# Optimization experiments

Hardware: AMD Instinct MI355X
Metric: run time of the kernel (lower is better)

The kernel has to match this reference:

```python
import jax, jax.numpy as jnp
import numpy as np

D_MODEL = 1024
RANK = 256
N_HEADS = 8
D_HEAD = RANK // N_HEADS
N_COMPRESS = 64
N_EXPAND = 64
N_KNOWLEDGE = 8192
COMPRESS_TOP_K = 8
EXPAND_TOP_K = 4
KNOWLEDGE_K = 8
B, S = 4, 512
NEG_INF = -1e9


def setup_inputs() -> dict:
    key = jax.random.key(0)
    ks = jax.random.split(key, 12)
    inp = {
        'x': jax.random.normal(ks[0], (B, S, D_MODEL), jnp.float32),
        'mask': jnp.tril(jnp.ones((S, S), bool))[None, None],  # [1,1,S,S] causal
        'compress_neurons': jax.random.normal(ks[1], (N_COMPRESS, D_MODEL, RANK), jnp.float32) / np.sqrt(D_MODEL),
        'expand_neurons': jax.random.normal(ks[2], (N_EXPAND, RANK, D_MODEL), jnp.float32) / np.sqrt(RANK),
        'knowledge_K': jax.random.normal(ks[3], (N_KNOWLEDGE, RANK), jnp.float32) * 0.02,
        'knowledge_V': jax.random.normal(ks[4], (N_KNOWLEDGE, D_MODEL), jnp.float32) * 0.02,
        'rq_w': jax.random.normal(ks[5], (N_COMPRESS, D_MODEL), jnp.float32) / np.sqrt(D_MODEL),
        'rk_w': jax.random.normal(ks[6], (N_COMPRESS, D_MODEL), jnp.float32) / np.sqrt(D_MODEL),
        'rv_w': jax.random.normal(ks[7], (N_COMPRESS, D_MODEL), jnp.float32) / np.sqrt(D_MODEL),
        'ro_w': jax.random.normal(ks[8], (N_EXPAND, RANK), jnp.float32) / np.sqrt(RANK),
        'rm_w': jax.random.normal(ks[9], (N_COMPRESS, D_MODEL), jnp.float32) / np.sqrt(D_MODEL),
        'g1': jnp.ones((D_MODEL,), jnp.float32),
        'b1': jnp.zeros((D_MODEL,), jnp.float32),
        'g2': jnp.ones((D_MODEL,), jnp.float32),
        'b2': jnp.zeros((D_MODEL,), jnp.float32),
    }
    return inp


def layernorm(x, g, b, eps=1e-5):
    mu = jnp.mean(x, -1, keepdims=True)
    var = jnp.mean((x - mu) ** 2, -1, keepdims=True)
    return (x - mu) * jax.lax.rsqrt(var + eps) * g + b


def compress(x, router_w, neurons, top_k):
    # x: [B,S,D]; neurons: [N,D,R]. Gather-then-matmul == matmul-then-gather.
    scores = jnp.einsum('bsd,nd->bsn', x, router_w)
    topk_scores, topk_idx = jax.lax.top_k(scores, top_k)
    w = jax.nn.softmax(topk_scores, -1)                          # [B,S,k]
    proj = jnp.einsum('bsd,ndr->bsnr', x, neurons)               # [B,S,N,R]
    sel = jnp.take_along_axis(proj, topk_idx[..., None], axis=2)  # [B,S,k,R]
    return jnp.sum(sel * w[..., None], axis=2)                   # [B,S,R]


def expand(x, router_w, neurons, top_k):
    # x: [B,S,R]; neurons: [N,R,D]
    scores = jnp.einsum('bsr,nr->bsn', x, router_w)
    topk_scores, topk_idx = jax.lax.top_k(scores, top_k)
    w = jax.nn.softmax(topk_scores, -1)
    proj = jnp.einsum('bsr,nrd->bsnd', x, neurons)               # [B,S,N,D]
    sel = jnp.take_along_axis(proj, topk_idx[..., None], axis=2)  # [B,S,k,D]
    return jnp.sum(sel * w[..., None], axis=2)                   # [B,S,D]


def reference(x, mask, compress_neurons, expand_neurons, knowledge_K, knowledge_V,
              rq_w, rk_w, rv_w, ro_w, rm_w, g1, b1, g2, b2):
    b, s, d = x.shape
    # --- attention sub-block (NeuronCircuit), pre-LN residual ---
    h = layernorm(x, g1, b1)
    Q = compress(h, rq_w, compress_neurons, COMPRESS_TOP_K)
    K = compress(h, rk_w, compress_neurons, COMPRESS_TOP_K)
    V = compress(h, rv_w, compress_neurons, COMPRESS_TOP_K)
    Q = Q.reshape(b, s, N_HEADS, D_HEAD).transpose(0, 2, 1, 3)
    K = K.reshape(b, s, N_HEADS, D_HEAD).transpose(0, 2, 1, 3)
    V = V.reshape(b, s, N_HEADS, D_HEAD).transpose(0, 2, 1, 3)
    att = jnp.einsum('bhqd,bhkd->bhqk', Q, K) / np.sqrt(D_HEAD)
    att = jnp.where(mask, att, NEG_INF)
    att = jax.nn.softmax(att, -1)
    attn_out = jnp.einsum('bhqk,bhkd->bhqd', att, V)
    attn_out = attn_out.transpose(0, 2, 1, 3).reshape(b, s, RANK)
    attn_out = expand(attn_out, ro_w, expand_neurons, EXPAND_TOP_K)
    x1 = x + attn_out
    # --- memory sub-block (NeuronMemory) ---
    h2 = layernorm(x1, g2, b2)
    Qm = compress(h2, rm_w, compress_neurons, COMPRESS_TOP_K)    # [B,S,R]
    kscores = jnp.einsum('bsr,nr->bsn', Qm, knowledge_K) / np.sqrt(RANK)
    k_top, k_idx = jax.lax.top_k(kscores, KNOWLEDGE_K)
    kw = jax.nn.softmax(k_top, -1)                               # [B,S,kk]
    sel_V = knowledge_V[k_idx]                                   # [B,S,kk,D]
    mem_out = jnp.sum(sel_V * kw[..., None], axis=2)
    return x1 + mem_out
```

## Files before the change

### kernel.cpp

```cpp
#include <hip/hip_runtime.h>

#define BS   2048
#define DM   1024
#define RK   256
#define NKN  8192
#define CK   8
#define EK   4
#define KK   8
#define KCH  32

#define NEGINF -1e30f

typedef __attribute__((ext_vector_type(8))) short short8;
typedef __attribute__((ext_vector_type(4))) float f32x4;

__device__ __forceinline__ unsigned short bf16_rtn(float v) {
  unsigned bits = __float_as_uint(v);
  return (unsigned short)((bits + 0x7fffu + ((bits >> 16) & 1u)) >> 16);
}
__device__ __forceinline__ float bf16f(unsigned short u) {
  return __uint_as_float(((unsigned)u) << 16);
}
__device__ __forceinline__ void split2(float v, unsigned short& h, unsigned short& l) {
  h = bf16_rtn(v);
  l = bf16_rtn(v - bf16f(h));
}

template<int TOPK>
__device__ inline void wave_topk64(float bv, int lane, float* tops, int* tidx) {
  #pragma unroll
  for (int k = 0; k < TOPK; ++k) {
    float mv = bv; int mp = lane;
    #pragma unroll
    for (int off = 32; off > 0; off >>= 1) {
      float ov = __shfl_xor(mv, off); int op = __shfl_xor(mp, off);
      if (ov > mv || (ov == mv && op < mp)) { mv = ov; mp = op; }
    }
    tops[k] = mv; tidx[k] = mp;
    if (lane == mp) bv = NEGINF;
  }
}

template<int TOPK>
__device__ inline void router_commit(int token, const float* tops, const int* tidx,
    float* w_out, int* lists, int* counts) {
  float mx = tops[0], se = 0.f, ex[TOPK];
  #pragma unroll
  for (int k = 0; k < TOPK; ++k) { ex[k] = expf(tops[k] - mx); se += ex[k]; }
  float inv = 1.f / se;
  #pragma unroll
  for (int k = 0; k < TOPK; ++k) {
    w_out[token*TOPK + k] = ex[k] * inv;
    int pos = atomicAdd(&counts[tidx[k]], 1);
    lists[tidx[k]*BS + pos] = token*TOPK + k;
  }
}

__global__ __launch_bounds__(256) void cvt_rwT(const float* __restrict__ rw,
                                               float* __restrict__ rwT, int dim4) {
  int i = blockIdx.x*256 + threadIdx.x;
  if (i >= 64*dim4) return;
  int n = i / dim4, jg = i % dim4;
  float4 v = *reinterpret_cast<const float4*>(rw + (size_t)n*dim4*4 + jg*4);
  *reinterpret_cast<float4*>(rwT + (size_t)jg*256 + n*4) = v;
}

__global__ __launch_bounds__(256) void ln_router3(const float* __restrict__ xin,
    const float* __restrict__ g, const float* __restrict__ bb,
    unsigned short* __restrict__ hh, unsigned short* __restrict__ hl,
    const float* __restrict__ w0T, const float* __restrict__ w1T, const float* __restrict__ w2T,
    float* __restrict__ w_all, int* __restrict__ lists, int* __restrict__ counts) {
  int row = blockIdx.x, t = threadIdx.x;
  __shared__ float red[256];
  __shared__ __align__(16) float hrow[DM];
  __shared__ float part[3][4][64];
  const float4 v = *reinterpret_cast<const float4*>(xin + (size_t)row*DM + t*4);
  red[t] = v.x + v.y + v.z + v.w;
  __syncthreads();
  for (int o = 128; o > 0; o >>= 1) { if (t < o) red[t] += red[t+o]; __syncthreads(); }
  float mu = red[0] * (1.f/DM);
  __syncthreads();
  float dx = v.x-mu, dy = v.y-mu, dz = v.z-mu, dw = v.w-mu;
  red[t] = dx*dx + dy*dy + dz*dz + dw*dw;
  __syncthreads();
  for (int o = 128; o > 0; o >>= 1) { if (t < o) red[t] += red[t+o]; __syncthreads(); }
  float rs = rsqrtf(red[0]*(1.f/DM) + 1e-5f);
  float4 gv = *reinterpret_cast<const float4*>(g + t*4);
  float4 bv = *reinterpret_cast<const float4*>(bb + t*4);
  float4 o4 = make_float4(dx*rs*gv.x+bv.x, dy*rs*gv.y+bv.y, dz*rs*gv.z+bv.z, dw*rs*gv.w+bv.w);
  ushort4 uh, ul;
  split2(o4.x, uh.x, ul.x); split2(o4.y, uh.y, ul.y);
  split2(o4.z, uh.z, ul.z); split2(o4.w, uh.w, ul.w);
  *reinterpret_cast<ushort4*>(hh + (size_t)row*DM + t*4) = uh;
  *reinterpret_cast<ushort4*>(hl + (size_t)row*DM + t*4) = ul;
  *reinterpret_cast<float4*>(&hrow[t*4]) = o4;
  __syncthreads();
  int n = t & 63, c = t >> 6;
  const float4* b0p = reinterpret_cast<const float4*>(w0T) + (size_t)c*64*64 + n;
  const float4* b1p = reinterpret_cast<const float4*>(w1T) + (size_t)c*64*64 + n;
  const float4* b2p = reinterpret_cast<const float4*>(w2T) + (size_t)c*64*64 + n;
  float p0 = 0.f, p1 = 0.f, p2 = 0.f;
  #pragma unroll 8
  for (int jg = 0; jg < 64; ++jg) {
    float4 a  = *reinterpret_cast<const float4*>(&hrow[(c*64 + jg)*4]);
    float4 b0 = b0p[(size_t)jg*64];
    float4 b1 = b1p[(size_t)jg*64];
    float4 b2 = b2p[(size_t)jg*64];
    p0 += a.x*b0.x + a.y*b0.y + a.z*b0.z + a.w*b0.w;
    p1 += a.x*b1.x + a.y*b1.y + a.z*b1.z + a.w*b1.w;
    p2 += a.x*b2.x + a.y*b2.y + a.z*b2.z + a.w*b2.w;
  }
  part[0][c][n] = p0; part[1][c][n] = p1; part[2][c][n] = p2;
  __syncthreads();
  int wv = t >> 6, lane = t & 63;
  if (wv < 3) {
    float bvv = part[wv][0][lane] + part[wv][1][lane] + part[wv][2][lane] + part[wv][3][lane];
    float tops[CK]; int tidx[CK];
    wave_topk64<CK>(bvv, lane, tops, tidx);
    if (lane == 0)
      router_commit<CK>(row, tops, tidx, w_all + (size_t)wv*BS*CK,
                        lists + (size_t)wv*64*BS, counts + wv*64);
  }
}

__global__ __launch_bounds__(256) void ln_router1(const float* __restrict__ xin,
    const float* __restrict__ g, const float* __restrict__ bb,
    unsigned short* __restrict__ hh, unsigned short* __restrict__ hl,
    const float* __restrict__ rwT,
    float* __restrict__ w_out, int* __restrict__ lists, int* __restrict__ counts) {
  int row = blockIdx.x, t = threadIdx.x;
  __shared__ float red[256];
  __shared__ __align__(16) float hrow[DM];
  __shared__ float part[4][64];
  const float4 v = *reinterpret_cast<const float4*>(xin + (size_t)row*DM + t*4);
  red[t] = v.x + v.y + v.z + v.w;
  __syncthreads();
  for (int o = 128; o > 0; o >>= 1) { if (t < o) red[t] += red[t+o]; __syncthreads(); }
  float mu = red[0] * (1.f/DM);
  __syncthreads();
  float dx = v.x-mu, dy = v.y-mu, dz = v.z-mu, dw = v.w-mu;
  red[t] = dx*dx + dy*dy + dz*dz + dw*dw;
  __syncthreads();
  for (int o = 128; o > 0; o >>= 1) { if (t < o) red[t] += red[t+o]; __syncthreads(); }
  float rs = rsqrtf(red[0]*(1.f/DM) + 1e-5f);
  float4 gv = *reinterpret_cast<const float4*>(g + t*4);
  float4 bv = *reinterpret_cast<const float4*>(bb + t*4);
  float4 o4 = make_float4(dx*rs*gv.x+bv.x, dy*rs*gv.y+bv.y, dz*rs*gv.z+bv.z, dw*rs*gv.w+bv.w);
  ushort4 uh, ul;
  split2(o4.x, uh.x, ul.x); split2(o4.y, uh.y, ul.y);
  split2(o4.z, uh.z, ul.z); split2(o4.w, uh.w, ul.w);
  *reinterpret_cast<ushort4*>(hh + (size_t)row*DM + t*4) = uh;
  *reinterpret_cast<ushort4*>(hl + (size_t)row*DM + t*4) = ul;
  *reinterpret_cast<float4*>(&hrow[t*4]) = o4;
  __syncthreads();
  int n = t & 63, c = t >> 6;
  const float4* bp = reinterpret_cast<const float4*>(rwT) + (size_t)c*64*64 + n;
  float p = 0.f;
  #pragma unroll 8
  for (int jg = 0; jg < 64; ++jg) {
    float4 a = *reinterpret_cast<const float4*>(&hrow[(c*64 + jg)*4]);
    float4 b = bp[(size_t)jg*64];
    p += a.x*b.x + a.y*b.y + a.z*b.z + a.w*b.w;
  }
  part[c][n] = p;
  __syncthreads();
  if (t < 64) {
    float bvv = part[0][t] + part[1][t] + part[2][t] + part[3][t];
    float tops[CK]; int tidx[CK];
    wave_topk64<CK>(bvv, t, tops, tidx);
    if (t == 0) router_commit<CK>(row, tops, tidx, w_out, lists, counts);
  }
}

template<int DIM, int TOPK>
__global__ __launch_bounds__(256) void router_topkT(const float* __restrict__ xin,
    const float* __restrict__ rwT, float* __restrict__ w_out,
    int* __restrict__ lists, int* __restrict__ counts) {
  int token = blockIdx.x, t = threadIdx.x;
  __shared__ __align__(16) float xrow[DIM];
  __shared__ float part[4][64];
  for (int i = t; i < DIM/4; i += 256)
    *reinterpret_cast<float4*>(&xrow[i*4]) =
        *reinterpret_cast<const float4*>(xin + (size_t)token*DIM + i*4);
  __syncthreads();
  int n = t & 63, c = t >> 6;
  const int JG = DIM / 16;
  const float4* bp = reinterpret_cast<const float4*>(rwT) + (size_t)c*JG*64 + n;
  float p = 0.f;
  #pragma unroll 8
  for (int jg = 0; jg < JG; ++jg) {
    float4 a = *reinterpret_cast<const float4*>(&xrow[(c*JG + jg)*4]);
    float4 b = bp[(size_t)jg*64];
    p += a.x*b.x + a.y*b.y + a.z*b.z + a.w*b.w;
  }
  part[c][n] = p;
  __syncthreads();
  if (t < 64) {
    float bv = part[0][t] + part[1][t] + part[2][t] + part[3][t];
    float tops[TOPK]; int tidx[TOPK];
    wave_topk64<TOPK>(bv, t, tops, tidx);
    if (t == 0) router_commit<TOPK>(token, tops, tidx, w_out, lists, counts);
  }
}

__global__ __launch_bounds__(256) void cvt_cnT(const float* __restrict__ cn,
    unsigned short* __restrict__ th, unsigned short* __restrict__ tl) {
  __shared__ float tile[32][33];
  int kb = blockIdx.x*32, cb = blockIdx.y*32, e = blockIdx.z;
  int tx = threadIdx.x & 31, ty = threadIdx.x >> 5;
  const size_t ebase = (size_t)e * DM * RK;
  for (int r = ty; r < 32; r += 8)
    tile[r][tx] = cn[ebase + (size_t)(kb + r)*RK + cb + tx];
  __syncthreads();
  for (int r = ty; r < 32; r += 8) {
    float v = tile[tx][r];
    unsigned short h, l; split2(v, h, l);
    size_t o = (size_t)e*RK*DM + (size_t)(cb + r)*DM + kb + tx;
    th[o] = h; tl[o] = l;
  }
}

__global__ __launch_bounds__(256) void ggemm_mfma(
    const unsigned short* __restrict__ xh, const unsigned short* __restrict__ xl,
    const unsigned short* __restrict__ WTh, const unsigned short* __restrict__ WTl,
    const float* __restrict__ w_all, const int* __restrict__ lists,
    const int* __restrict__ counts, float* __restrict__ out) {
  int e = blockIdx.x, which = blockIdx.z;
  int cnt = counts[which*64 + e];
  int base = blockIdx.y * 64;
  if (base >= cnt) return;
  const int* list_e = lists + ((size_t)which*64 + e)*BS;
  const float* wvp = w_all + (size_t)which*BS*CK;
  int t = threadIdx.x, w = t >> 6, l = t & 63, lr = l & 15, lg = l >> 4;
  __shared__ int   toks[64];
  __shared__ float wts[64];
  if (t < 64) {
    int idx = base + t;
    if (idx < cnt) { int e2 = list_e[idx]; toks[t] = e2 / CK; wts[t] = wvp[e2]; }
    else           { toks[t] = -1; wts[t] = 0.f; }
  }
  __syncthreads();
  f32x4 acc[4][4];
  #pragma unroll
  for (int mi = 0; mi < 4; ++mi)
    #pragma unroll
    for (int ni = 0; ni < 4; ++ni) acc[mi][ni] = (f32x4)0.f;
  const unsigned short* Ahb = WTh + ((size_t)e*RK + w*64 + lr)*DM + lg*8;
  const unsigned short* Alb = WTl + ((size_t)e*RK + w*64 + lr)*DM + lg*8;
  int tokn[4]; float wtn[4];
  const unsigned short *Bh[4], *Bl[4];
  #pragma unroll
  for (int ni = 0; ni < 4; ++ni) {
    tokn[ni] = toks[ni*16 + lr];
    wtn[ni]  = wts[ni*16 + lr];
    int tk = tokn[ni] >= 0 ? tokn[ni] : 0;
    Bh[ni] = xh + (size_t)tk*DM + lg*8;
    Bl[ni] = xl + (size_t)tk*DM + lg*8;
  }
  for (int k0 = 0; k0 < DM; k0 += 32) {
    short8 ah[4], al[4], bh[4], bl[4];
    #pragma unroll
    for (int mi = 0; mi < 4; ++mi) {
      ah[mi] = *reinterpret_cast<const short8*>(Ahb + (size_t)mi*16*DM + k0);
      al[mi] = *reinterpret_cast<const short8*>(Alb + (size_t)mi*16*DM + k0);
    }
    #pragma unroll
    for (int ni = 0; ni < 4; ++ni) {
      bh[ni] = *reinterpret_cast<const short8*>(Bh[ni] + k0);
      bl[ni] = *reinterpret_cast<const short8*>(Bl[ni] + k0);
    }
    #pragma unroll
    for (int mi = 0; mi < 4; ++mi)
      #pragma unroll
      for (int ni = 0; ni < 4; ++ni) {
        acc[mi][ni] = __builtin_amdgcn_mfma_f32_16x16x32_bf16(ah[mi], bh[ni], acc[mi][ni], 0, 0, 0);
        acc[mi][ni] = __builtin_amdgcn_mfma_f32_16x16x32_bf16(ah[mi], bl[ni], acc[mi][ni], 0, 0, 0);
        acc[mi][ni] = __builtin_amdgcn_mfma_f32_16x16x32_bf16(al[mi], bh[ni], acc[mi][ni], 0, 0, 0);
      }
  }
  #pragma unroll
  for (int ni = 0; ni < 4; ++ni) {
    if (tokn[ni] < 0) continue;
    float wt = wtn[ni];
    float* orow = out + ((size_t)which*BS + tokn[ni])*RK;
    #pragma unroll
    for (int mi = 0; mi < 4; ++mi) {
      int col = w*64 + mi*16 + lg*4;
      #pragma unroll
      for (int r = 0; r < 4; ++r)
        atomicAdd(&orow[col + r], wt * acc[mi][ni][r]);
    }
  }
}

template<int KDIM, int NCOLT, int TK>
__global__ __launch_bounds__(256) void ggemm_f32(const float* __restrict__ xin,
    const float* __restrict__ neurons, const float* __restrict__ w_all,
    const int* __restrict__ lists, const int* __restrict__ counts,
    float* __restrict__ out) {
  constexpr int COLCH = NCOLT / 256;
  int e = blockIdx.x;
  int which = blockIdx.z / COLCH, cc = blockIdx.z % COLCH;
  int cnt = counts[which*64 + e];
  int base = blockIdx.y * 64;
  if (base >= cnt) return;
  const int* list_e = lists + ((size_t)which*64 + e)*BS;
  const float* wvp = w_all + (size_t)which*BS*TK;
  int t = threadIdx.x;
  __shared__ __align__(16) float Bs[16][256];
  __shared__ __align__(16) float At[16][64];
  __shared__ int   toks[64];
  __shared__ float wts[64];
  if (t < 64) {
    int idx = base + t;
    if (idx < cnt) { int e2 = list_e[idx]; toks[t] = e2 / TK; wts[t] = wvp[e2]; }
    else           { toks[t] = -1; wts[t] = 0.f; }
  }
  __syncthreads();
  float acc[8][8];
  #pragma unroll
  for (int i = 0; i < 8; ++i)
    #pragma unroll
    for (int j = 0; j < 8; ++j) acc[i][j] = 0.f;
  int tr = t >> 5, tc = t & 31;
  const float* W = neurons + (size_t)e*KDIM*NCOLT + cc*256;
  int ar = t & 63, akc = (t >> 6) * 4;
  int tokA = toks[ar];
  const float* Arow = xin + (size_t)(tokA >= 0 ? tokA : 0)*KDIM + akc;

  for (int k0 = 0; k0 < KDIM; k0 += 16) {
    float4 b0r, b1r, b2r, b3r;
    {
      int f0 = t*4;
      b0r = *reinterpret_cast<const float4*>(W + (size_t)(k0 + (f0>>8))*NCOLT + (f0&255));
      int f1 = 1024 + t*4;
      b1r = *reinterpret_cast<const float4*>(W + (size_t)(k0 + (f1>>8))*NCOLT + (f1&255));
      int f2 = 2048 + t*4;
      b2r = *reinterpret_cast<const float4*>(W + (size_t)(k0 + (f2>>8))*NCOLT + (f2&255));
      int f3 = 3072 + t*4;
      b3r = *reinterpret_cast<const float4*>(W + (size_t)(k0 + (f3>>8))*NCOLT + (f3&255));
    }
    float4 av = *reinterpret_cast<const float4*>(Arow + k0);
    if (tokA < 0) av = make_float4(0.f, 0.f, 0.f, 0.f);
    __syncthreads();
    {
      int f0 = t*4;
      *reinterpret_cast<float4*>(&Bs[0][0] + f0)        = b0r;
      *reinterpret_cast<float4*>(&Bs[0][0] + f0 + 1024) = b1r;
      *reinterpret_cast<float4*>(&Bs[0][0] + f0 + 2048) = b2r;
      *reinterpret_cast<float4*>(&Bs[0][0] + f0 + 3072) = b3r;
      At[akc+0][ar] = av.x; At[akc+1][ar] = av.y;
      At[akc+2][ar] = av.z; At[akc+3][ar] = av.w;
    }
    __syncthreads();
    #pragma unroll
    for (int kk = 0; kk < 16; ++kk) {
      float4 a0 = *reinterpret_cast<const float4*>(&At[kk][tr*8]);
      float4 a1 = *reinterpret_cast<const float4*>(&At[kk][tr*8 + 4]);
      float4 p0 = *reinterpret_cast<const float4*>(&Bs[kk][tc*4]);
      float4 p1 = *reinterpret_cast<const float4*>(&Bs[kk][128 + tc*4]);
      float a[8] = {a0.x,a0.y,a0.z,a0.w,a1.x,a1.y,a1.z,a1.w};
      float b[8] = {p0.x,p0.y,p0.z,p0.w,p1.x,p1.y,p1.z,p1.w};
      #pragma unroll
      for (int i = 0; i < 8; ++i)
        #pragma unroll
        for (int j = 0; j < 8; ++j)
          acc[i][j] = fmaf(a[i], b[j], acc[i][j]);
    }
  }
  #pragma unroll
  for (int i = 0; i < 8; ++i) {
    int r = tr*8 + i;
    int tok = toks[r];
    if (tok < 0) continue;
    float wt = wts[r];
    float* orow = out + ((size_t)which*BS + tok)*NCOLT + cc*256;
    #pragma unroll
    for (int j = 0; j < 4; ++j) {
      atomicAdd(&orow[tc*4 + j],       wt * acc[i][j]);
      atomicAdd(&orow[128 + tc*4 + j], wt * acc[i][j+4]);
    }
  }
}

__global__ __launch_bounds__(256) void attn_kernel(const float* __restrict__ Q,
    const float* __restrict__ K, const float* __restrict__ V, float* __restrict__ AO) {
  int qs = blockIdx.x;
  int hb = blockIdx.y; int h = hb & 7, b = hb >> 3;
  int t = threadIdx.x;
  __shared__ float qv[32];
  __shared__ float sc[512];
  __shared__ float red[256];
  const size_t baseQ = ((size_t)(b*512 + qs))*RK + h*32;
  if (t < 32) qv[t] = Q[baseQ + t];
  __syncthreads();
  int nk = qs + 1;
  const float scale = 0.17677669529663687f;
  for (int k = t; k < nk; k += 256) {
    const float* kr = K + ((size_t)(b*512 + k))*RK + h*32;
    float s = 0.f;
    #pragma unroll
    for (int d = 0; d < 32; d += 4) {
      float4 kv = *reinterpret_cast<const float4*>(kr + d);
      s += kv.x*qv[d] + kv.y*qv[d+1] + kv.z*qv[d+2] + kv.w*qv[d+3];
    }
    sc[k] = s * scale;
  }
  __syncthreads();
  float m = NEGINF;
  for (int k = t; k < nk; k += 256) m = fmaxf(m, sc[k]);
  red[t] = m; __syncthreads();
  for (int o = 128; o > 0; o >>= 1) { if (t < o) red[t] = fmaxf(red[t], red[t+o]); __syncthreads(); }
  m = red[0];
  __syncthreads();
  float sloc = 0.f;
  for (int k = t; k < nk; k += 256) { float pp = expf(sc[k] - m); sc[k] = pp; sloc += pp; }
  red[t] = sloc; __syncthreads();
  for (int o = 128; o > 0; o >>= 1) { if (t < o) red[t] += red[t+o]; __syncthreads(); }
  float inv = 1.f / red[0];
  __syncthreads();
  int d = t & 31, c = t >> 5;
  float pa = 0.f;
  for (int k = c; k < nk; k += 8)
    pa += sc[k] * V[((size_t)(b*512 + k))*RK + h*32 + d];
  red[c*32 + d] = pa; __syncthreads();
  if (t < 32) {
    float o = 0.f;
    #pragma unroll
    for (int c2 = 0; c2 < 8; ++c2) o += red[c2*32 + t];
    AO[baseQ + t] = o * inv;
  }
}

__global__ __launch_bounds__(256) void f2bf(const float* __restrict__ in,
                                            unsigned short* __restrict__ out, int n8) {
  int i = blockIdx.x*256 + threadIdx.x;
  if (i >= n8) return;
  float4 a = reinterpret_cast<const float4*>(in)[2*i];
  float4 b = reinterpret_cast<const float4*>(in)[2*i + 1];
  float v[8] = {a.x,a.y,a.z,a.w,b.x,b.y,b.z,b.w};
  unsigned u[8];
  #pragma unroll
  for (int j = 0; j < 8; ++j) {
    unsigned bits = __float_as_uint(v[j]);
    u[j] = (bits + 0x7fffu + ((bits >> 16) & 1u)) >> 16;
  }
  uint4 o;
  o.x = u[0] | (u[1] << 16); o.y = u[2] | (u[3] << 16);
  o.z = u[4] | (u[5] << 16); o.w = u[6] | (u[7] << 16);
  *reinterpret_cast<uint4*>(out + 8*i) = o;
}

__global__ __launch_bounds__(256) void kscore_mfma(const unsigned short* __restrict__ Qmb,
    const unsigned short* __restrict__ kKb, float* __restrict__ cand_s, int* __restrict__ cand_i) {
  int tile = blockIdx.x, chunk = blockIdx.y;
  int t = threadIdx.x, w = t >> 6, l = t & 63;
  int lr = l & 15, lg = l >> 4;
  __shared__ float sc[32][265];
  f32x4 acc[4][2];
  #pragma unroll
  for (int mi = 0; mi < 4; ++mi)
    #pragma unroll
    for (int ti = 0; ti < 2; ++ti) acc[mi][ti] = (f32x4)0.f;
  const unsigned short* Abase = kKb + ((size_t)(chunk*256 + w*64 + lr))*RK + lg*8;
  const unsigned short* Bbase = Qmb + ((size_t)(tile*32 + lr))*RK + lg*8;
  #pragma unroll
  for (int k0 = 0; k0 < RK; k0 += 32) {
    short8 af[4], bf[2];
    #pragma unroll
    for (int mi = 0; mi < 4; ++mi)
      af[mi] = *reinterpret_cast<const short8*>(Abase + (size_t)mi*16*RK + k0);
    #pragma unroll
    for (int ti = 0; ti < 2; ++ti)
      bf[ti] = *reinterpret_cast<const short8*>(Bbase + (size_t)ti*16*RK + k0);
    #pragma unroll
    for (int mi = 0; mi < 4; ++mi)
      #pragma unroll
      for (int ti = 0; ti < 2; ++ti)
        acc[mi][ti] = __builtin_amdgcn_mfma_f32_16x16x32_bf16(af[mi], bf[ti], acc[mi][ti], 0, 0, 0);
  }
  #pragma unroll
  for (int mi = 0; mi < 4; ++mi)
    #pragma unroll
    for (int ti = 0; ti < 2; ++ti)
      #pragma unroll
      for (int r = 0; r < 4; ++r)
        sc[ti*16 + lr][w*64 + mi*16 + lg*4 + r] = acc[mi][ti][r];
  __syncthreads();
  for (int s = 0; s < 8; ++s) {
    int tok = w*8 + s;
    float v0 = sc[tok][l], v1 = sc[tok][l+64], v2 = sc[tok][l+128], v3 = sc[tok][l+192];
    size_t cbase = ((size_t)(tile*32 + tok)*KCH + chunk)*KK;
    #pragma unroll
    for (int iter = 0; iter < KK; ++iter) {
      float mv = v0; int mp = l;
      if (v1 > mv) { mv = v1; mp = l+64; }
      if (v2 > mv) { mv = v2; mp = l+128; }
      if (v3 > mv) { mv = v3; mp = l+192; }
      #pragma unroll
      for (int off = 32; off > 0; off >>= 1) {
        float ov = __shfl_xor(mv, off); int op = __shfl_xor(mp, off);
        if (ov > mv || (ov == mv && op < mp)) { mv = ov; mp = op; }
      }
      if ((mp & 63) == l) {
        int j = mp >> 6;
        if (j == 0) v0 = NEGINF; else if (j == 1) v1 = NEGINF;
        else if (j == 2) v2 = NEGINF; else v3 = NEGINF;
      }
      if (l == 0) { cand_s[cbase + iter] = mv; cand_i[cbase + iter] = chunk*256 + mp; }
    }
  }
}

__global__ __launch_bounds__(256) void knowledge_merge(const float* __restrict__ cand_s,
    const int* __restrict__ cand_i, const float* __restrict__ kV, float* __restrict__ xout) {
  int tok = blockIdx.x, t = threadIdx.x;
  __shared__ float s_sc[256];
  __shared__ int   s_ix[256];
  __shared__ float w8[KK];
  __shared__ int   i8[KK];
  s_sc[t] = cand_s[(size_t)tok*256 + t];
  s_ix[t] = cand_i[(size_t)tok*256 + t];
  __syncthreads();
  if (t < 64) {
    float v0 = s_sc[t], v1 = s_sc[t+64], v2 = s_sc[t+128], v3 = s_sc[t+192];
    float tops[KK]; int tpos[KK];
    #pragma unroll
    for (int iter = 0; iter < KK; ++iter) {
      float mv = v0; int mp = t;
      if (v1 > mv) { mv = v1; mp = t+64; }
      if (v2 > mv) { mv = v2; mp = t+128; }
      if (v3 > mv) { mv = v3; mp = t+192; }
      #pragma unroll
      for (int off = 32; off > 0; off >>= 1) {
        float ov = __shfl_xor(mv, off); int op = __shfl_xor(mp, off);
        if (ov > mv || (ov == mv && op < mp)) { mv = ov; mp = op; }
      }
      tops[iter] = mv; tpos[iter] = mp;
      if ((mp & 63) == t) {
        int j = mp >> 6;
        if (j == 0) v0 = NEGINF; else if (j == 1) v1 = NEGINF;
        else if (j == 2) v2 = NEGINF; else v3 = NEGINF;
      }
    }
    if (t == 0) {
      const float kscale = 1.f/16.f;
      float mx = tops[0]*kscale, se = 0.f, ex[KK];
      #pragma unroll
      for (int k = 0; k < KK; ++k) { ex[k] = expf(tops[k]*kscale - mx); se += ex[k]; }
      float inv = 1.f / se;
      #pragma unroll
      for (int k = 0; k < KK; ++k) { w8[k] = ex[k]*inv; i8[k] = s_ix[tpos[k]]; }
    }
  }
  __syncthreads();
  size_t orow = (size_t)tok * DM;
  float4 o = *reinterpret_cast<const float4*>(xout + orow + t*4);
  #pragma unroll
  for (int k = 0; k < KK; ++k) {
    float w = w8[k];
    const float4 v4 = *reinterpret_cast<const float4*>(kV + (size_t)i8[k]*DM + t*4);
    o.x += w*v4.x; o.y += w*v4.y; o.z += w*v4.z; o.w += w*v4.w;
  }
  *reinterpret_cast<float4*>(xout + orow + t*4) = o;
}

extern "C" void kernel_launch(void* const* d_in, const int* in_sizes, int n_in,
                              void* d_out, int out_size, void* d_ws, size_t ws_size,
                              hipStream_t stream) {
  const float* x  = (const float*)d_in[0];
  const float* cn = (const float*)d_in[2];
  const float* en = (const float*)d_in[3];
  const float* kK = (const float*)d_in[4];
  const float* kV = (const float*)d_in[5];
  const float* rq = (const float*)d_in[6];
  const float* rk = (const float*)d_in[7];
  const float* rv = (const float*)d_in[8];
  const float* ro = (const float*)d_in[9];
  const float* rm = (const float*)d_in[10];
  const float* g1 = (const float*)d_in[11];
  const float* b1 = (const float*)d_in[12];
  const float* g2 = (const float*)d_in[13];
  const float* b2 = (const float*)d_in[14];
  float* out = (float*)d_out;

  char* p = (char*)d_ws;
  auto alloc = [&](size_t bytes) { char* r = p; p += (bytes + 255) & ~(size_t)255; return r; };
  unsigned short* h_h  = (unsigned short*)alloc((size_t)BS*DM*2);
  unsigned short* h_l  = (unsigned short*)alloc((size_t)BS*DM*2);
  unsigned short* h2_h = (unsigned short*)alloc((size_t)BS*DM*2);
  unsigned short* h2_l = (unsigned short*)alloc((size_t)BS*DM*2);
  unsigned short* cnT_h = (unsigned short*)alloc((size_t)64*RK*DM*2);
  unsigned short* cnT_l = (unsigned short*)alloc((size_t)64*RK*DM*2);
  float* rqT  = (float*)alloc((size_t)64*DM*4);
  float* rkT  = (float*)alloc((size_t)64*DM*4);
  float* rvT  = (float*)alloc((size_t)64*DM*4);
  float* rmT  = (float*)alloc((size_t)64*DM*4);
  float* roT  = (float*)alloc((size_t)64*RK*4);
  float* Q    = (float*)alloc((size_t)BS*RK*4);
  float* Kb   = (float*)alloc((size_t)BS*RK*4);
  float* Vb   = (float*)alloc((size_t)BS*RK*4);
  float* Qm   = (float*)alloc((size_t)BS*RK*4);
  float* AO   = (float*)alloc((size_t)BS*RK*4);
  float* w_all= (float*)alloc((size_t)3*BS*CK*4);
  float* w_o  = (float*)alloc((size_t)BS*EK*4);
  float* w_m  = (float*)alloc((size_t)BS*CK*4);
  float* cand_s = (float*)alloc((size_t)BS*KCH*KK*4);
  int*   cand_i = (int*)  alloc((size_t)BS*KCH*KK*4);
  unsigned short* Qmb = (unsigned short*)alloc((size_t)BS*RK*2);
  unsigned short* kKb = (unsigned short*)alloc((size_t)NKN*RK*2);
  int* lists  = (int*)alloc((size_t)5*64*BS*4);
  int* counts = (int*)alloc((size_t)5*64*4);

  int *listo = lists + 3*64*BS, *listm = lists + 4*64*BS;
  int *co = counts + 192, *cm = counts + 256;

  hipMemsetAsync(counts, 0, 5*64*4, stream);
  hipMemsetAsync(Q, 0, (size_t)BS*RK*4*4, stream);

  cvt_rwT<<<64, 256, 0, stream>>>(rq, rqT, DM/4);
  cvt_rwT<<<64, 256, 0, stream>>>(rk, rkT, DM/4);
  cvt_rwT<<<64, 256, 0, stream>>>(rv, rvT, DM/4);
  cvt_rwT<<<64, 256, 0, stream>>>(rm, rmT, DM/4);
  cvt_rwT<<<16, 256, 0, stream>>>(ro, roT, RK/4);
  cvt_cnT<<<dim3(32, 8, 64), 256, 0, stream>>>(cn, cnT_h, cnT_l);
  f2bf<<<NKN*RK/8/256, 256, 0, stream>>>(kK, kKb, NKN*RK/8);

  ln_router3<<<BS, 256, 0, stream>>>(x, g1, b1, h_h, h_l, rqT, rkT, rvT, w_all, lists, counts);
  ggemm_mfma<<<dim3(64, 16, 3), 256, 0, stream>>>(h_h, h_l, cnT_h, cnT_l,
                                                  w_all, lists, counts, Q);

  attn_kernel<<<dim3(512, 32), 256, 0, stream>>>(Q, Kb, Vb, AO);

  hipMemcpyAsync(out, x, (size_t)BS*DM*4, hipMemcpyDeviceToDevice, stream);

  router_topkT<RK, EK><<<BS, 256, 0, stream>>>(AO, roT, w_o, listo, co);
  ggemm_f32<RK, DM, EK><<<dim3(64, 16, 4), 256, 0, stream>>>(AO, en, w_o, listo, co, out);

  ln_router1<<<BS, 256, 0, stream>>>(out, g2, b2, h2_h, h2_l, rmT, w_m, listm, cm);
  ggemm_mfma<<<dim3(64, 16, 1), 256, 0, stream>>>(h2_h, h2_l, cnT_h, cnT_l,
                                                  w_m, listm, cm, Qm);

  f2bf<<<BS*RK/8/256, 256, 0, stream>>>(Qm, Qmb, BS*RK/8);
  kscore_mfma<<<dim3(BS/32, KCH), 256, 0, stream>>>(Qmb, kKb, cand_s, cand_i);
  knowledge_merge<<<BS, 256, 0, stream>>>(cand_s, cand_i, kV, out);
}
```

Measured before the change: 1.437 ms.

## Merge Q/K/V router lists per expert so one grouped GEMM tile serves all three

The three compress routers (Q, K, V) now write into a single per-expert list with a shared counter, and each entry encodes which projection it belongs to. The grouped MFMA GEMM then reads one combined list per expert rather than three separate lists. This packs tokens from all three projections into full 64-row tiles and reuses each expert's weight tile across them, so fewer blocks run partially filled. In exchange, the atomic counter per expert sees three times the contention and the token index has to be decoded with bit tricks.

```diff
diff --git a/kernel.cpp b/kernel.cpp
--- a/kernel.cpp
+++ b/kernel.cpp
@@ -8,6 +8,7 @@
 #define EK   4
 #define KK   8
 #define KCH  32
+#define LSTR (3*BS)
 
 #define NEGINF -1e30f
 
@@ -43,7 +44,7 @@
 
 template<int TOPK>
 __device__ inline void router_commit(int token, const float* tops, const int* tidx,
-    float* w_out, int* lists, int* counts) {
+    float* w_out, int entoff, int* lists, int lstr, int* counts) {
   float mx = tops[0], se = 0.f, ex[TOPK];
   #pragma unroll
   for (int k = 0; k < TOPK; ++k) { ex[k] = expf(tops[k] - mx); se += ex[k]; }
@@ -52,7 +53,7 @@
   for (int k = 0; k < TOPK; ++k) {
     w_out[token*TOPK + k] = ex[k] * inv;
     int pos = atomicAdd(&counts[tidx[k]], 1);
-    lists[tidx[k]*BS + pos] = token*TOPK + k;
+    lists[tidx[k]*lstr + pos] = entoff + token*TOPK + k;
   }
 }
 
@@ -69,7 +70,7 @@
     const float* __restrict__ g, const float* __restrict__ bb,
     unsigned short* __restrict__ hh, unsigned short* __restrict__ hl,
     const float* __restrict__ w0T, const float* __restrict__ w1T, const float* __restrict__ w2T,
-    float* __restrict__ w_all, int* __restrict__ lists, int* __restrict__ counts) {
+    float* __restrict__ w_all, int* __restrict__ listc, int* __restrict__ ccomb) {
   int row = blockIdx.x, t = threadIdx.x;
   __shared__ float red[256];
   __shared__ __align__(16) float hrow[DM];
@@ -118,8 +119,8 @@
     float tops[CK]; int tidx[CK];
     wave_topk64<CK>(bvv, lane, tops, tidx);
     if (lane == 0)
-      router_commit<CK>(row, tops, tidx, w_all + (size_t)wv*BS*CK,
-                        lists + (size_t)wv*64*BS, counts + wv*64);
+      router_commit<CK>(row, tops, tidx, w_all + (size_t)wv*BS*CK, wv*BS*CK,
+                        listc, LSTR, ccomb);
   }
 }
 
@@ -168,7 +169,7 @@
     float bvv = part[0][t] + part[1][t] + part[2][t] + part[3][t];
     float tops[CK]; int tidx[CK];
     wave_topk64<CK>(bvv, t, tops, tidx);
-    if (t == 0) router_commit<CK>(row, tops, tidx, w_out, lists, counts);
+    if (t == 0) router_commit<CK>(row, tops, tidx, w_out, 0, lists, BS, counts);
   }
 }
 
@@ -199,7 +200,7 @@
     float bv = part[0][t] + part[1][t] + part[2][t] + part[3][t];
     float tops[TOPK]; int tidx[TOPK];
     wave_topk64<TOPK>(bv, t, tops, tidx);
-    if (t == 0) router_commit<TOPK>(token, tops, tidx, w_out, lists, counts);
+    if (t == 0) router_commit<TOPK>(token, tops, tidx, w_out, 0, lists, BS, counts);
   }
 }
 
@@ -223,21 +224,24 @@
 __global__ __launch_bounds__(256) void ggemm_mfma(
     const unsigned short* __restrict__ xh, const unsigned short* __restrict__ xl,
     const unsigned short* __restrict__ WTh, const unsigned short* __restrict__ WTl,
-    const float* __restrict__ w_all, const int* __restrict__ lists,
-    const int* __restrict__ counts, float* __restrict__ out) {
-  int e = blockIdx.x, which = blockIdx.z;
-  int cnt = counts[which*64 + e];
-  int base = blockIdx.y * 64;
+    const float* __restrict__ w_all, const int* __restrict__ listc, int lstr,
+    const int* __restrict__ ccomb, float* __restrict__ out) {
+  int gid = blockIdx.x;
+  int e = gid & 63;
+  int base = (gid >> 6) * 64;
+  int cnt = ccomb[e];
   if (base >= cnt) return;
-  const int* list_e = lists + ((size_t)which*64 + e)*BS;
-  const float* wvp = w_all + (size_t)which*BS*CK;
+  const int* list_e = listc + (size_t)e*lstr;
   int t = threadIdx.x, w = t >> 6, l = t & 63, lr = l & 15, lg = l >> 4;
   __shared__ int   toks[64];
   __shared__ float wts[64];
   if (t < 64) {
     int idx = base + t;
-    if (idx < cnt) { int e2 = list_e[idx]; toks[t] = e2 / CK; wts[t] = wvp[e2]; }
-    else           { toks[t] = -1; wts[t] = 0.f; }
+    if (idx < cnt) {
+      int ent = list_e[idx];
+      toks[t] = (ent >> 14)*BS + ((ent & 16383) >> 3);
+      wts[t]  = w_all[ent];
+    } else { toks[t] = -1; wts[t] = 0.f; }
   }
   __syncthreads();
   f32x4 acc[4][4];
@@ -253,7 +257,7 @@
   for (int ni = 0; ni < 4; ++ni) {
     tokn[ni] = toks[ni*16 + lr];
     wtn[ni]  = wts[ni*16 + lr];
-    int tk = tokn[ni] >= 0 ? tokn[ni] : 0;
+    int tk = tokn[ni] >= 0 ? (tokn[ni] & (BS-1)) : 0;
     Bh[ni] = xh + (size_t)tk*DM + lg*8;
     Bl[ni] = xl + (size_t)tk*DM + lg*8;
   }
@@ -282,7 +286,7 @@
   for (int ni = 0; ni < 4; ++ni) {
     if (tokn[ni] < 0) continue;
     float wt = wtn[ni];
-    float* orow = out + ((size_t)which*BS + tokn[ni])*RK;
+    float* orow = out + (size_t)tokn[ni]*RK;
     #pragma unroll
     for (int mi = 0; mi < 4; ++mi) {
       int col = w*64 + mi*16 + lg*4;
@@ -609,13 +613,14 @@
   int*   cand_i = (int*)  alloc((size_t)BS*KCH*KK*4);
   unsigned short* Qmb = (unsigned short*)alloc((size_t)BS*RK*2);
   unsigned short* kKb = (unsigned short*)alloc((size_t)NKN*RK*2);
-  int* lists  = (int*)alloc((size_t)5*64*BS*4);
-  int* counts = (int*)alloc((size_t)5*64*4);
-
-  int *listo = lists + 3*64*BS, *listm = lists + 4*64*BS;
-  int *co = counts + 192, *cm = counts + 256;
-
-  hipMemsetAsync(counts, 0, 5*64*4, stream);
+  int* listc  = (int*)alloc((size_t)64*LSTR*4);
+  int* listo  = (int*)alloc((size_t)64*BS*4);
+  int* listm  = (int*)alloc((size_t)64*BS*4);
+  int* counts = (int*)alloc((size_t)3*64*4);
+
+  int *ccomb = counts, *co = counts + 64, *cm = counts + 128;
+
+  hipMemsetAsync(counts, 0, 3*64*4, stream);
   hipMemsetAsync(Q, 0, (size_t)BS*RK*4*4, stream);
 
   cvt_rwT<<<64, 256, 0, stream>>>(rq, rqT, DM/4);
@@ -626,9 +631,9 @@
   cvt_cnT<<<dim3(32, 8, 64), 256, 0, stream>>>(cn, cnT_h, cnT_l);
   f2bf<<<NKN*RK/8/256, 256, 0, stream>>>(kK, kKb, NKN*RK/8);
 
-  ln_router3<<<BS, 256, 0, stream>>>(x, g1, b1, h_h, h_l, rqT, rkT, rvT, w_all, lists, counts);
-  ggemm_mfma<<<dim3(64, 16, 3), 256, 0, stream>>>(h_h, h_l, cnT_h, cnT_l,
-                                                  w_all, lists, counts, Q);
+  ln_router3<<<BS, 256, 0, stream>>>(x, g1, b1, h_h, h_l, rqT, rkT, rvT, w_all, listc, ccomb);
+  ggemm_mfma<<<64*(LSTR/64), 256, 0, stream>>>(h_h, h_l, cnT_h, cnT_l,
+                                               w_all, listc, LSTR, ccomb, Q);
 
   attn_kernel<<<dim3(512, 32), 256, 0, stream>>>(Q, Kb, Vb, AO);
 
@@ -638,8 +643,8 @@
   ggemm_f32<RK, DM, EK><<<dim3(64, 16, 4), 256, 0, stream>>>(AO, en, w_o, listo, co, out);
 
   ln_router1<<<BS, 256, 0, stream>>>(out, g2, b2, h2_h, h2_l, rmT, w_m, listm, cm);
-  ggemm_mfma<<<dim3(64, 16, 1), 256, 0, stream>>>(h2_h, h2_l, cnT_h, cnT_l,
-                                                  w_m, listm, cm, Qm);
+  ggemm_mfma<<<64*(BS/64), 256, 0, stream>>>(h2_h, h2_l, cnT_h, cnT_l,
+                                             w_m, listm, BS, cm, Qm);
 
   f2bf<<<BS*RK/8/256, 256, 0, stream>>>(Qm, Qmb, BS*RK/8);
   kscore_mfma<<<dim3(BS/32, KCH), 256, 0, stream>>>(Qmb, kKb, cand_s, cand_i);
```

Measured after the change: 1.614 ms. +12.3%, slower.
